# Kernel tuning notes

Measured on AMD Instinct MI355X. Metric: run time of the kernel, lower is better.

The kernel has to match this reference:

```python
import jax, jax.numpy as jnp
import numpy as np

LN_EPS = 1e-5


def setup_inputs() -> dict:
    key = jax.random.key(0)
    ks = jax.random.split(key, 6)
    B, M, N, D = 16, 128, 128, 128
    NM, H = 16, 512
    xav = float(np.sqrt(2.0 / (D + D)))  # xavier_normal over (in_dim, out_dim) fan
    return {
        "x": jax.random.normal(ks[0], (B, M, N, D), jnp.float32),
        "w1": jax.random.normal(ks[1], (D, D, NM, 2), jnp.float32) * xav,
        "w2": jax.random.normal(ks[2], (D, D, NM, 2), jnp.float32) * xav,
        "ff_w0": jax.random.normal(ks[3], (D, H), jnp.float32) * float(1.0 / np.sqrt(D)),
        "ff_b0": jnp.zeros((H,), jnp.float32),
        "ff_w1": jax.random.normal(ks[4], (H, D), jnp.float32) * float(1.0 / np.sqrt(H)),
        "ff_b1": jnp.zeros((D,), jnp.float32),
        "ln_g": jnp.ones((D,), jnp.float32),
        "ln_b": jnp.zeros((D,), jnp.float32),
    }


def _layer_norm(h, g, b):
    mu = jnp.mean(h, axis=-1, keepdims=True)
    var = jnp.mean(jnp.square(h - mu), axis=-1, keepdims=True)
    return (h - mu) * jax.lax.rsqrt(var + LN_EPS) * g + b


def _forward_fourier(x, w1, w2):
    # x: [B, M, N, I] -> [B, I, M, N]
    xt = jnp.transpose(x, (0, 3, 1, 2))
    B, I, M, N = xt.shape
    nm = w1.shape[2]
    cw1 = w1[..., 0] + 1j * w1[..., 1]  # [I, O, nm]
    cw2 = w2[..., 0] + 1j * w2[..., 1]
    O = cw1.shape[1]

    # Fourier along last axis (y)
    fty = jnp.fft.rfft(xt, axis=-1, norm="ortho")                    # [B,I,M,N//2+1]
    f1 = jnp.einsum("bixy,ioy->boxy", fty[..., :nm], cw1)            # [B,O,M,nm]
    pad_y = jnp.zeros((B, O, M, N // 2 + 1 - nm), dtype=f1.dtype)
    xy = jnp.fft.irfft(jnp.concatenate([f1, pad_y], axis=-1), n=N, axis=-1, norm="ortho")

    # Fourier along second-to-last axis (x)
    ftx = jnp.fft.rfft(xt, axis=-2, norm="ortho")                    # [B,I,M//2+1,N]
    f2 = jnp.einsum("bixy,iox->boxy", ftx[:, :, :nm, :], cw2)        # [B,O,nm,N]
    pad_x = jnp.zeros((B, O, M // 2 + 1 - nm, N), dtype=f2.dtype)
    xx = jnp.fft.irfft(jnp.concatenate([f2, pad_x], axis=-2), n=M, axis=-2, norm="ortho")

    return jnp.transpose(xx + xy, (0, 2, 3, 1))  # [B,M,N,O]


def reference(x, w1, w2, ff_w0, ff_b0, ff_w1, ff_b1, ln_g, ln_b):
    h = _forward_fourier(x, w1, w2)
    # backcast FeedForward: Linear -> ReLU -> Linear -> LayerNorm (dropout=0)
    h1 = jax.nn.relu(jnp.einsum("bmni,ih->bmnh", h, ff_w0) + ff_b0)
    h2 = jnp.einsum("bmnh,ho->bmno", h1, ff_w1) + ff_b1
    return _layer_norm(h2, ln_g, ln_b)
```

## Files before the change

kernel.cpp:

```cpp
#include <hip/hip_runtime.h>


#define LN_EPS 1e-5f
#define NMODES 16
#define FROW 4096
#define HROW 16384

typedef __attribute__((ext_vector_type(8))) short short8;
typedef __attribute__((ext_vector_type(8))) ushort ushort8;
typedef __attribute__((ext_vector_type(4))) ushort ushort4v;
typedef __attribute__((ext_vector_type(4))) short short4v;
typedef __attribute__((ext_vector_type(4))) float f32x4;

__device__ __forceinline__ ushort f2bf(float f) {
    unsigned u = __float_as_uint(f);
    unsigned r = (u + 0x7FFFu + ((u >> 16) & 1u)) >> 16;
    return (ushort)r;
}
__device__ __forceinline__ float bf2f(ushort h) {
    return __uint_as_float(((unsigned)h) << 16);
}

__global__ void k_setup(float* __restrict__ Tc, float* __restrict__ Ts,
                        float* __restrict__ IT) {
    const float invs = 0.08838834764831845f;
    for (int idx = threadIdx.x; idx < NMODES * 128; idx += blockDim.x) {
        int k = idx >> 7, n = idx & 127;
        int p = (k * n) & 127;
        float th = (float)p * (6.283185307179586f / 128.0f);
        float c = cosf(th), s = sinf(th);
        Tc[idx] = c * invs;
        Ts[idx] = -s * invs;
        float ck = (k == 0) ? invs : 2.0f * invs;
        IT[n * 32 + 2 * k]     = ck * c;
        IT[n * 32 + 2 * k + 1] = -ck * s;
    }
}

__global__ void k_wpack(const float* __restrict__ w, ushort* __restrict__ Wph,
                        ushort* __restrict__ Wpl) {
    int idx = blockIdx.x * 256 + threadIdx.x;
    int k  = idx >> 16;
    int op = (idx >> 8) & 255;
    int ip = idx & 255;
    int i = ip & 127, o = op & 127;
    const float* base = w + (((i << 7) | o) * NMODES + k) * 2;
    float re = base[0], im = base[1];
    float v = (ip < 128) ? ((op < 128) ? re : im)
                         : ((op < 128) ? -im : re);
    ushort hi = f2bf(v);
    ushort lo = f2bf(v - bf2f(hi));
    Wph[idx] = hi;
    Wpl[idx] = lo;
}

__global__ __launch_bounds__(256) void k_wcvt(const float* __restrict__ w0,
        const float* __restrict__ w1, ushort* __restrict__ w0t,
        ushort* __restrict__ w1t) {
    int idx = blockIdx.x * 256 + threadIdx.x;
    int h = idx >> 7, k = idx & 127;
    w0t[idx] = f2bf(w0[k * 512 + h]);
    int o = idx >> 9, hh = idx & 511;
    w1t[idx] = f2bf(w1[hh * 128 + o]);
}

__global__ __launch_bounds__(128) void k_fft(const float* __restrict__ x,
        const float* __restrict__ Tc, const float* __restrict__ Ts,
        float* __restrict__ F, int mode) {
    __shared__ float Tc_s[NMODES * 128];
    __shared__ float Ts_s[NMODES * 128];
    for (int e = threadIdx.x; e < NMODES * 128; e += 128) {
        Tc_s[e] = Tc[e];
        Ts_s[e] = Ts[e];
    }
    __syncthreads();
    int row = blockIdx.x * 4 + (threadIdx.x >> 5);
    int i0 = (threadIdx.x & 31) * 4;
    size_t base; int ts;
    if (mode == 0) { base = (size_t)row * HROW; ts = 128; }
    else { base = (size_t)(row >> 7) * 2097152 + (size_t)(row & 127) * 128; ts = 16384; }

    f32x4 re[NMODES], im[NMODES];
#pragma unroll
    for (int k = 0; k < NMODES; ++k) {
        re[k] = {0.f, 0.f, 0.f, 0.f};
        im[k] = {0.f, 0.f, 0.f, 0.f};
    }

    f32x4 xv[4];
#pragma unroll
    for (int j = 0; j < 4; ++j)
        xv[j] = *(const f32x4*)(x + base + (size_t)j * ts + i0);

#pragma unroll 1
    for (int tb = 0; tb < 32; ++tb) {
        int t0 = tb * 4;
        f32x4 nx[4];
        if (tb < 31) {
#pragma unroll
            for (int j = 0; j < 4; ++j)
                nx[j] = *(const f32x4*)(x + base + (size_t)(t0 + 4 + j) * ts + i0);
        }
#pragma unroll
        for (int k = 0; k < NMODES; ++k) {
            f32x4 c4 = *(const f32x4*)&Tc_s[k * 128 + t0];
            f32x4 s4 = *(const f32x4*)&Ts_s[k * 128 + t0];
#pragma unroll
            for (int q = 0; q < 4; ++q) {
                re[k][q] += xv[0][q] * c4[0] + xv[1][q] * c4[1]
                          + xv[2][q] * c4[2] + xv[3][q] * c4[3];
                im[k][q] += xv[0][q] * s4[0] + xv[1][q] * s4[1]
                          + xv[2][q] * s4[2] + xv[3][q] * s4[3];
            }
        }
        if (tb < 31) {
#pragma unroll
            for (int j = 0; j < 4; ++j) xv[j] = nx[j];
        }
    }
    float* outp = F + (size_t)row * FROW;
#pragma unroll
    for (int k = 0; k < NMODES; ++k) {
        *(f32x4*)(outp + k * 256 + i0)       = re[k];
        *(f32x4*)(outp + k * 256 + 128 + i0) = im[k];
    }
}

__global__ __launch_bounds__(256) void k_mixm(const float* __restrict__ A,
        const ushort* __restrict__ Wph, const ushort* __restrict__ Wpl,
        float* __restrict__ outF) {
    __shared__ ushort Ah[32 * 264];
    __shared__ ushort Al[32 * 264];
    int tid = threadIdx.x;
    int kt = blockIdx.x & 15;
    int bm0 = (blockIdx.x >> 4) * 32;
    {
        int row = tid >> 3, cg = tid & 7;
        const float* arow = A + (bm0 + row) * FROW + kt * 256 + cg * 32;
        ushort* ah = &Ah[row * 264 + cg * 32];
        ushort* al = &Al[row * 264 + cg * 32];
#pragma unroll
        for (int j = 0; j < 8; ++j) {
            f32x4 v = *(const f32x4*)(arow + j * 4);
            short4v h4, l4;
#pragma unroll
            for (int q = 0; q < 4; ++q) {
                ushort h = f2bf(v[q]);
                h4[q] = (short)h;
                l4[q] = (short)f2bf(v[q] - bf2f(h));
            }
            *(short4v*)(ah + j * 4) = h4;
            *(short4v*)(al + j * 4) = l4;
        }
    }
    __syncthreads();
    int lane = tid & 63, wid = tid >> 6;
    int frow = lane & 15, fk8 = (lane >> 4) * 8, fr4 = (lane >> 4) * 4;
    f32x4 acc[2][4];
#pragma unroll
    for (int a = 0; a < 2; ++a)
#pragma unroll
        for (int c = 0; c < 4; ++c) acc[a][c] = {0.f, 0.f, 0.f, 0.f};
    const ushort* wph = Wph + kt * 65536;
    const ushort* wpl = Wpl + kt * 65536;
#pragma unroll
    for (int kk = 0; kk < 8; ++kk) {
        short8 ah0 = *(const short8*)&Ah[(frow)      * 264 + kk * 32 + fk8];
        short8 ah1 = *(const short8*)&Ah[(16 + frow) * 264 + kk * 32 + fk8];
        short8 al0 = *(const short8*)&Al[(frow)      * 264 + kk * 32 + fk8];
        short8 al1 = *(const short8*)&Al[(16 + frow) * 264 + kk * 32 + fk8];
#pragma unroll
        for (int tc = 0; tc < 4; ++tc) {
            int op = wid * 64 + tc * 16 + frow;
            int base = op * 256 + kk * 32 + fk8;
            short8 wh = *(const short8*)&wph[base];
            short8 wl = *(const short8*)&wpl[base];
            acc[0][tc] = __builtin_amdgcn_mfma_f32_16x16x32_bf16(ah0, wh, acc[0][tc], 0, 0, 0);
            acc[0][tc] = __builtin_amdgcn_mfma_f32_16x16x32_bf16(ah0, wl, acc[0][tc], 0, 0, 0);
            acc[0][tc] = __builtin_amdgcn_mfma_f32_16x16x32_bf16(al0, wh, acc[0][tc], 0, 0, 0);
            acc[1][tc] = __builtin_amdgcn_mfma_f32_16x16x32_bf16(ah1, wh, acc[1][tc], 0, 0, 0);
            acc[1][tc] = __builtin_amdgcn_mfma_f32_16x16x32_bf16(ah1, wl, acc[1][tc], 0, 0, 0);
            acc[1][tc] = __builtin_amdgcn_mfma_f32_16x16x32_bf16(al1, wh, acc[1][tc], 0, 0, 0);
        }
    }
#pragma unroll
    for (int tr = 0; tr < 2; ++tr)
#pragma unroll
        for (int tc = 0; tc < 4; ++tc)
#pragma unroll
            for (int r = 0; r < 4; ++r)
                outF[(bm0 + tr * 16 + fr4 + r) * FROW + kt * 256 + wid * 64 + tc * 16 + frow]
                    = acc[tr][tc][r];
}

__global__ __launch_bounds__(1024) void k_icdft(const float* __restrict__ f,
        const float* __restrict__ IT, ushort* __restrict__ obf,
        float* __restrict__ h32, const ushort* __restrict__ hyin, int mode) {
    __shared__ float IT_s[128 * 32];
    __shared__ float f_s[32 * 128];
    int tid = threadIdx.x;
    int row = blockIdx.x;
    *(f32x4*)&IT_s[tid * 4] = *(const f32x4*)&IT[tid * 4];
    *(f32x4*)&f_s[tid * 4]  = *(const f32x4*)(f + (size_t)row * FROW + tid * 4);
    __syncthreads();
    int og = tid & 31, ng = tid >> 5;
    int o4 = og * 4;

    f32x4 acc[4];
#pragma unroll
    for (int j = 0; j < 4; ++j) acc[j] = {0.f, 0.f, 0.f, 0.f};

#pragma unroll
    for (int kpb = 0; kpb < 8; ++kpb) {
        int kp0 = kpb * 4;
        f32x4 fv0 = *(const f32x4*)&f_s[(kp0 + 0) * 128 + o4];
        f32x4 fv1 = *(const f32x4*)&f_s[(kp0 + 1) * 128 + o4];
        f32x4 fv2 = *(const f32x4*)&f_s[(kp0 + 2) * 128 + o4];
        f32x4 fv3 = *(const f32x4*)&f_s[(kp0 + 3) * 128 + o4];
#pragma unroll
        for (int j = 0; j < 4; ++j) {
            int n = ng * 4 + j;
            f32x4 it = *(const f32x4*)&IT_s[n * 32 + kp0];
#pragma unroll
            for (int q = 0; q < 4; ++q)
                acc[j][q] += fv0[q] * it[0] + fv1[q] * it[1]
                           + fv2[q] * it[2] + fv3[q] * it[3];
        }
    }

    if (mode == 0) {
#pragma unroll
        for (int j = 0; j < 4; ++j) {
            int n = ng * 4 + j;
            ushort4v t;
#pragma unroll
            for (int q = 0; q < 4; ++q) t[q] = f2bf(acc[j][q]);
            *(ushort4v*)&obf[(size_t)row * HROW + n * 128 + o4] = t;
        }
    } else if (mode == 1) {
#pragma unroll
        for (int j = 0; j < 4; ++j) {
            int n = ng * 4 + j;
            *(f32x4*)&h32[(size_t)row * HROW + n * 128 + o4] = acc[j];
        }
    } else if (mode == 2) {
        size_t base = (size_t)(row >> 7) * 2097152 + (size_t)(row & 127) * 128 + o4;
#pragma unroll
        for (int j = 0; j < 4; ++j) {
            int n = ng * 4 + j;
            size_t ix = base + (size_t)n * 16384;
            ushort4v hv = *(const ushort4v*)&hyin[ix];
            ushort4v t;
#pragma unroll
            for (int q = 0; q < 4; ++q) t[q] = f2bf(bf2f(hv[q]) + acc[j][q]);
            *(ushort4v*)&obf[ix] = t;
        }
    } else {
        size_t base = (size_t)(row >> 7) * 2097152 + (size_t)(row & 127) * 128 + o4;
#pragma unroll
        for (int j = 0; j < 4; ++j) {
            int n = ng * 4 + j;
            size_t ix = base + (size_t)n * 16384;
            f32x4 hv = *(const f32x4*)&h32[ix];
            ushort4v t;
#pragma unroll
            for (int q = 0; q < 4; ++q) t[q] = f2bf(hv[q] + acc[j][q]);
            *(ushort4v*)&obf[ix] = t;
        }
    }
}

__global__ __launch_bounds__(256) void k_ffn1(const ushort* __restrict__ hin,
        const ushort* __restrict__ w0t, const float* __restrict__ b0,
        ushort* __restrict__ h1o) {
    __shared__ ushort A_l[128 * 136];
    __shared__ ushort B_l[64 * 136];
    int tid = threadIdx.x;
    int ht = blockIdx.x & 7, rt = blockIdx.x >> 3;
    int R0 = rt * 128, H0 = ht * 64;

#pragma unroll
    for (int i = 0; i < 8; ++i) {
        int e = tid + i * 256;
        int row = e >> 4, c16 = e & 15;
        *(ushort8*)&A_l[row * 136 + c16 * 8] =
            *(const ushort8*)(hin + (size_t)(R0 + row) * 128 + c16 * 8);
    }
#pragma unroll
    for (int i = 0; i < 4; ++i) {
        int e = tid + i * 256;
        int row = e >> 4, c16 = e & 15;
        *(ushort8*)&B_l[row * 136 + c16 * 8] =
            *(const ushort8*)(w0t + (H0 + row) * 128 + c16 * 8);
    }
    __syncthreads();

    int lane = tid & 63, wave = tid >> 6;
    int frow = lane & 15, qg = lane >> 4, fk8 = qg * 8, fr4 = qg * 4;
    int r2 = wave >> 1, c2 = wave & 1;

    f32x4 acc[4][2];
#pragma unroll
    for (int a = 0; a < 4; ++a)
#pragma unroll
        for (int c = 0; c < 2; ++c) acc[a][c] = {0.f, 0.f, 0.f, 0.f};

#pragma unroll
    for (int kk = 0; kk < 4; ++kk) {
        short8 af[4], bf[2];
#pragma unroll
        for (int tr = 0; tr < 4; ++tr)
            af[tr] = *(const short8*)&A_l[(r2 * 64 + tr * 16 + frow) * 136 + kk * 32 + fk8];
#pragma unroll
        for (int tc = 0; tc < 2; ++tc)
            bf[tc] = *(const short8*)&B_l[(c2 * 32 + tc * 16 + frow) * 136 + kk * 32 + fk8];
#pragma unroll
        for (int tr = 0; tr < 4; ++tr)
#pragma unroll
            for (int tc = 0; tc < 2; ++tc)
                acc[tr][tc] = __builtin_amdgcn_mfma_f32_16x16x32_bf16(
                    af[tr], bf[tc], acc[tr][tc], 0, 0, 0);
    }

    float b0v[2];
    b0v[0] = b0[H0 + c2 * 32 + frow];
    b0v[1] = b0[H0 + c2 * 32 + 16 + frow];
#pragma unroll
    for (int tr = 0; tr < 4; ++tr)
#pragma unroll
        for (int tc = 0; tc < 2; ++tc)
#pragma unroll
            for (int r = 0; r < 4; ++r) {
                int row = r2 * 64 + tr * 16 + fr4 + r;
                int col = H0 + c2 * 32 + tc * 16 + frow;
                h1o[(size_t)(R0 + row) * 512 + col] =
                    f2bf(fmaxf(acc[tr][tc][r] + b0v[tc], 0.f));
            }
}

__global__ __launch_bounds__(256) void k_ffn2(const ushort* __restrict__ h1,
        const ushort* __restrict__ w1t, const float* __restrict__ b1,
        const float* __restrict__ g, const float* __restrict__ bb,
        float* __restrict__ out) {
    __shared__ ushort A_l[32 * 72];
    __shared__ ushort B_l[128 * 72];
    __shared__ float ps_s[128];
    __shared__ float pq_s[128];
    int tid = threadIdx.x;
    int R0 = blockIdx.x * 32;
    int lane = tid & 63, wave = tid >> 6;
    int frow = lane & 15, qg = lane >> 4, fk8 = qg * 8, fr4 = qg * 4;
    int sAr = tid >> 3, sc8 = tid & 7;

    *(ushort8*)&A_l[sAr * 72 + sc8 * 8] =
        *(const ushort8*)(h1 + (size_t)(R0 + sAr) * 512 + sc8 * 8);
#pragma unroll
    for (int i = 0; i < 4; ++i) {
        int ro = sAr + i * 32;
        *(ushort8*)&B_l[ro * 72 + sc8 * 8] =
            *(const ushort8*)(w1t + ro * 512 + sc8 * 8);
    }
    __syncthreads();

    f32x4 acc[2][2];
#pragma unroll
    for (int a = 0; a < 2; ++a)
#pragma unroll
        for (int c = 0; c < 2; ++c) acc[a][c] = {0.f, 0.f, 0.f, 0.f};

#pragma unroll 1
    for (int kt = 0; kt < 8; ++kt) {
        ushort8 sa, sb0, sb1, sb2, sb3;
        if (kt < 7) {
            int koff = (kt + 1) * 64 + sc8 * 8;
            sa  = *(const ushort8*)(h1 + (size_t)(R0 + sAr) * 512 + koff);
            sb0 = *(const ushort8*)(w1t + (sAr +  0) * 512 + koff);
            sb1 = *(const ushort8*)(w1t + (sAr + 32) * 512 + koff);
            sb2 = *(const ushort8*)(w1t + (sAr + 64) * 512 + koff);
            sb3 = *(const ushort8*)(w1t + (sAr + 96) * 512 + koff);
        }
#pragma unroll
        for (int kk = 0; kk < 2; ++kk) {
            short8 af[2], bf[2];
#pragma unroll
            for (int tr = 0; tr < 2; ++tr)
                af[tr] = *(const short8*)&A_l[(tr * 16 + frow) * 72 + kk * 32 + fk8];
#pragma unroll
            for (int tc = 0; tc < 2; ++tc)
                bf[tc] = *(const short8*)&B_l[(wave * 32 + tc * 16 + frow) * 72 + kk * 32 + fk8];
#pragma unroll
            for (int tr = 0; tr < 2; ++tr)
#pragma unroll
                for (int tc = 0; tc < 2; ++tc)
                    acc[tr][tc] = __builtin_amdgcn_mfma_f32_16x16x32_bf16(
                        af[tr], bf[tc], acc[tr][tc], 0, 0, 0);
        }
        __syncthreads();
        if (kt < 7) {
            *(ushort8*)&A_l[sAr * 72 + sc8 * 8] = sa;
            *(ushort8*)&B_l[(sAr +  0) * 72 + sc8 * 8] = sb0;
            *(ushort8*)&B_l[(sAr + 32) * 72 + sc8 * 8] = sb1;
            *(ushort8*)&B_l[(sAr + 64) * 72 + sc8 * 8] = sb2;
            *(ushort8*)&B_l[(sAr + 96) * 72 + sc8 * 8] = sb3;
            __syncthreads();
        }
    }

    float b1v[2], gv[2], bv[2];
#pragma unroll
    for (int tc = 0; tc < 2; ++tc) {
        int o = wave * 32 + tc * 16 + frow;
        b1v[tc] = b1[o]; gv[tc] = g[o]; bv[tc] = bb[o];
    }
#pragma unroll
    for (int tr = 0; tr < 2; ++tr)
#pragma unroll
        for (int r = 0; r < 4; ++r) {
            float s = 0.f, qq = 0.f;
#pragma unroll
            for (int tc = 0; tc < 2; ++tc) {
                float v = acc[tr][tc][r] + b1v[tc];
                acc[tr][tc][r] = v;
                s += v; qq += v * v;
            }
            s += __shfl_xor(s, 1); qq += __shfl_xor(qq, 1);
            s += __shfl_xor(s, 2); qq += __shfl_xor(qq, 2);
            s += __shfl_xor(s, 4); qq += __shfl_xor(qq, 4);
            s += __shfl_xor(s, 8); qq += __shfl_xor(qq, 8);
            if (frow == 0) {
                int row = tr * 16 + fr4 + r;
                ps_s[wave * 32 + row] = s;
                pq_s[wave * 32 + row] = qq;
            }
        }
    __syncthreads();
#pragma unroll
    for (int tr = 0; tr < 2; ++tr)
#pragma unroll
        for (int r = 0; r < 4; ++r) {
            int row = tr * 16 + fr4 + r;
            float S = ps_s[row] + ps_s[32 + row] + ps_s[64 + row] + ps_s[96 + row];
            float Q = pq_s[row] + pq_s[32 + row] + pq_s[64 + row] + pq_s[96 + row];
            float mu = S * (1.0f / 128.0f);
            float var = Q * (1.0f / 128.0f) - mu * mu;
            float rs = rsqrtf(fmaxf(var, 0.f) + LN_EPS);
            float* orow = &out[(size_t)(R0 + row) * 128 + wave * 32];
            orow[frow]      = (acc[tr][0][r] - mu) * rs * gv[0] + bv[0];
            orow[16 + frow] = (acc[tr][1][r] - mu) * rs * gv[1] + bv[1];
        }
}

extern "C" void kernel_launch(void* const* d_in, const int* in_sizes, int n_in,
                              void* d_out, int out_size, void* d_ws, size_t ws_size,
                              hipStream_t stream) {
    (void)in_sizes; (void)n_in; (void)out_size;
    const float* x   = (const float*)d_in[0];
    const float* w1  = (const float*)d_in[1];
    const float* w2  = (const float*)d_in[2];
    const float* fw0 = (const float*)d_in[3];
    const float* fb0 = (const float*)d_in[4];
    const float* fw1 = (const float*)d_in[5];
    const float* fb1 = (const float*)d_in[6];
    const float* lng = (const float*)d_in[7];
    const float* lnb = (const float*)d_in[8];
    float* out = (float*)d_out;

    char* ws = (char*)d_ws;
    float*  Tc  = (float*)(ws);
    float*  Ts  = (float*)(ws + 8192);
    float*  IT  = (float*)(ws + 16384);
    ushort* Wph = (ushort*)(ws + 32768);
    ushort* Wpl = (ushort*)(ws + 32768 + 2097152);
    ushort* w0t = (ushort*)(ws + 4227072);
    ushort* w1t = (ushort*)(ws + 4358144);
    float*  buf0 = (float*)(ws + 4489216);
    ushort* hy   = (ushort*)(ws + 38043648);
    ushort* hsum = (ushort*)(ws + 105152512);
    const size_t need_two = 172261376ull;
    int two = (ws_size >= need_two) ? 1 : 0;
    ushort* hbfs = hy;

    k_setup<<<1, 256, 0, stream>>>(Tc, Ts, IT);
    k_wcvt <<<256, 256, 0, stream>>>(fw0, fw1, w0t, w1t);

    k_wpack<<<4096, 256, 0, stream>>>(w1, Wph, Wpl);
    k_fft  <<<512, 128, 0, stream>>>(x, Tc, Ts, buf0, 0);
    k_mixm <<<1024, 256, 0, stream>>>(buf0, Wph, Wpl, buf0);
    if (two) k_icdft<<<2048, 1024, 0, stream>>>(buf0, IT, hy, out, hy, 0);
    else     k_icdft<<<2048, 1024, 0, stream>>>(buf0, IT, hy, out, hy, 1);

    k_wpack<<<4096, 256, 0, stream>>>(w2, Wph, Wpl);
    k_fft  <<<512, 128, 0, stream>>>(x, Tc, Ts, buf0, 1);
    k_mixm <<<1024, 256, 0, stream>>>(buf0, Wph, Wpl, buf0);
    if (two) k_icdft<<<2048, 1024, 0, stream>>>(buf0, IT, hsum, out, hy, 2);
    else     k_icdft<<<2048, 1024, 0, stream>>>(buf0, IT, hbfs, out, hy, 3);

    if (two) {
        for (int c = 0; c < 4; ++c) {
            const size_t off = (size_t)c * 65536 * 128;
            k_ffn1<<<4096, 256, 0, stream>>>(hsum + off, w0t, fb0, hy);
            k_ffn2<<<2048, 256, 0, stream>>>(hy, w1t, fb1, lng, lnb, out + off);
        }
    } else {
        ushort* h1buf = (ushort*)buf0;
        for (int c = 0; c < 8; ++c) {
            const size_t off = (size_t)c * 32768 * 128;
            k_ffn1<<<2048, 256, 0, stream>>>(hbfs + off, w0t, fb0, h1buf);
            k_ffn2<<<1024, 256, 0, stream>>>(h1buf, w1t, fb1, lng, lnb, out + off);
        }
    }
}
```

Before: 540.7 us.

## Compute truncated forward DFT with split-bf16 MFMA instead of scalar FMA

The forward partial DFT (16 modes, cos/sin) becomes a matrix multiply on MFMA 16x16x32 bf16 instructions. The twiddle table is stored as hi/lo bf16 pairs, and each slab of x is split into hi/lo bf16 in LDS, with three MFMAs per tile approximating fp32 accuracy. One block now handles one 128x128 slab instead of four rows per block. This replaces the scalar FMA-bound loop with matrix-core throughput, at the cost of split-precision error, extra LDS traffic and synchronisation.

```diff
diff --git a/kernel.cpp b/kernel.cpp
--- a/kernel.cpp
+++ b/kernel.cpp
@@ -21,19 +21,26 @@
     return __uint_as_float(((unsigned)h) << 16);
 }
 
-__global__ void k_setup(float* __restrict__ Tc, float* __restrict__ Ts,
+__global__ void k_setup(ushort* __restrict__ T2h, ushort* __restrict__ T2l,
                         float* __restrict__ IT) {
     const float invs = 0.08838834764831845f;
+    for (int idx = threadIdx.x; idx < 32 * 128; idx += blockDim.x) {
+        int kp = idx >> 7, n = idx & 127;
+        int k = kp >> 1;
+        int p = (k * n) & 127;
+        float th = (float)p * (6.283185307179586f / 128.0f);
+        float v = (kp & 1) ? (-sinf(th) * invs) : (cosf(th) * invs);
+        ushort hi = f2bf(v);
+        T2h[idx] = hi;
+        T2l[idx] = f2bf(v - bf2f(hi));
+    }
     for (int idx = threadIdx.x; idx < NMODES * 128; idx += blockDim.x) {
         int k = idx >> 7, n = idx & 127;
         int p = (k * n) & 127;
         float th = (float)p * (6.283185307179586f / 128.0f);
-        float c = cosf(th), s = sinf(th);
-        Tc[idx] = c * invs;
-        Ts[idx] = -s * invs;
         float ck = (k == 0) ? invs : 2.0f * invs;
-        IT[n * 32 + 2 * k]     = ck * c;
-        IT[n * 32 + 2 * k + 1] = -ck * s;
+        IT[n * 32 + 2 * k]     = ck * cosf(th);
+        IT[n * 32 + 2 * k + 1] = -ck * sinf(th);
     }
 }
 
@@ -64,66 +71,85 @@
     w1t[idx] = f2bf(w1[hh * 128 + o]);
 }
 
-__global__ __launch_bounds__(128) void k_fft(const float* __restrict__ x,
-        const float* __restrict__ Tc, const float* __restrict__ Ts,
+__global__ __launch_bounds__(256) void k_fft(const float* __restrict__ x,
+        const ushort* __restrict__ T2h, const ushort* __restrict__ T2l,
         float* __restrict__ F, int mode) {
-    __shared__ float Tc_s[NMODES * 128];
-    __shared__ float Ts_s[NMODES * 128];
-    for (int e = threadIdx.x; e < NMODES * 128; e += 128) {
-        Tc_s[e] = Tc[e];
-        Ts_s[e] = Ts[e];
-    }
-    __syncthreads();
-    int row = blockIdx.x * 4 + (threadIdx.x >> 5);
-    int i0 = (threadIdx.x & 31) * 4;
+    __shared__ ushort Xh[128 * 38];
+    __shared__ ushort Xl[128 * 38];
+    int tid = threadIdx.x;
+    int slab = blockIdx.x;
     size_t base; int ts;
-    if (mode == 0) { base = (size_t)row * HROW; ts = 128; }
-    else { base = (size_t)(row >> 7) * 2097152 + (size_t)(row & 127) * 128; ts = 16384; }
-
-    f32x4 re[NMODES], im[NMODES];
-#pragma unroll
-    for (int k = 0; k < NMODES; ++k) {
-        re[k] = {0.f, 0.f, 0.f, 0.f};
-        im[k] = {0.f, 0.f, 0.f, 0.f};
-    }
-
-    f32x4 xv[4];
-#pragma unroll
-    for (int j = 0; j < 4; ++j)
-        xv[j] = *(const f32x4*)(x + base + (size_t)j * ts + i0);
+    if (mode == 0) { base = (size_t)slab * HROW; ts = 128; }
+    else { base = (size_t)(slab >> 7) * 2097152 + (size_t)(slab & 127) * 128; ts = 16384; }
+
+    int sr2 = tid >> 4, sc = tid & 15;
+    int lane = tid & 63, w = tid >> 6;
+    int frow = lane & 15, fk8 = (lane >> 4) * 8, fr4 = (lane >> 4) * 4;
+
+    f32x4 acc[2][2];
+#pragma unroll
+    for (int a = 0; a < 2; ++a)
+#pragma unroll
+        for (int c = 0; c < 2; ++c) acc[a][c] = {0.f, 0.f, 0.f, 0.f};
 
 #pragma unroll 1
-    for (int tb = 0; tb < 32; ++tb) {
-        int t0 = tb * 4;
-        f32x4 nx[4];
-        if (tb < 31) {
-#pragma unroll
-            for (int j = 0; j < 4; ++j)
-                nx[j] = *(const f32x4*)(x + base + (size_t)(t0 + 4 + j) * ts + i0);
-        }
-#pragma unroll
-        for (int k = 0; k < NMODES; ++k) {
-            f32x4 c4 = *(const f32x4*)&Tc_s[k * 128 + t0];
-            f32x4 s4 = *(const f32x4*)&Ts_s[k * 128 + t0];
-#pragma unroll
-            for (int q = 0; q < 4; ++q) {
-                re[k][q] += xv[0][q] * c4[0] + xv[1][q] * c4[1]
-                          + xv[2][q] * c4[2] + xv[3][q] * c4[3];
-                im[k][q] += xv[0][q] * s4[0] + xv[1][q] * s4[1]
-                          + xv[2][q] * s4[2] + xv[3][q] * s4[3];
+    for (int nc = 0; nc < 4; ++nc) {
+        if (nc) __syncthreads();
+        {
+            const float* pa = x + base + (size_t)(nc * 32 + 2 * sr2) * ts + sc * 8;
+            const float* pb = pa + ts;
+            f32x4 a0 = *(const f32x4*)pa;
+            f32x4 a1 = *(const f32x4*)(pa + 4);
+            f32x4 b0 = *(const f32x4*)pb;
+            f32x4 b1 = *(const f32x4*)(pb + 4);
+            uint* xh32 = (uint*)Xh;
+            uint* xl32 = (uint*)Xl;
+#pragma unroll
+            for (int q = 0; q < 8; ++q) {
+                float av = (q < 4) ? a0[q] : a1[q - 4];
+                float bv = (q < 4) ? b0[q] : b1[q - 4];
+                ushort ah = f2bf(av), bh = f2bf(bv);
+                ushort al = f2bf(av - bf2f(ah)), bl = f2bf(bv - bf2f(bh));
+                int i = sc * 8 + q;
+                xh32[i * 19 + sr2] = (uint)ah | ((uint)bh << 16);
+                xl32[i * 19 + sr2] = (uint)al | ((uint)bl << 16);
             }
         }
-        if (tb < 31) {
-#pragma unroll
-            for (int j = 0; j < 4; ++j) xv[j] = nx[j];
-        }
-    }
-    float* outp = F + (size_t)row * FROW;
-#pragma unroll
-    for (int k = 0; k < NMODES; ++k) {
-        *(f32x4*)(outp + k * 256 + i0)       = re[k];
-        *(f32x4*)(outp + k * 256 + 128 + i0) = im[k];
-    }
+        __syncthreads();
+        short8 ah_[2], al_[2], bh_[2], bl_[2];
+#pragma unroll
+        for (int kt = 0; kt < 2; ++kt) {
+            int ro = (kt * 16 + frow) * 128 + nc * 32 + fk8;
+            ah_[kt] = *(const short8*)&T2h[ro];
+            al_[kt] = *(const short8*)&T2l[ro];
+        }
+#pragma unroll
+        for (int it = 0; it < 2; ++it) {
+            int i = w * 32 + it * 16 + frow;
+            bh_[it] = *(const short8*)&Xh[i * 38 + fk8];
+            bl_[it] = *(const short8*)&Xl[i * 38 + fk8];
+        }
+#pragma unroll
+        for (int kt = 0; kt < 2; ++kt)
+#pragma unroll
+            for (int it = 0; it < 2; ++it) {
+                acc[kt][it] = __builtin_amdgcn_mfma_f32_16x16x32_bf16(
+                    ah_[kt], bh_[it], acc[kt][it], 0, 0, 0);
+                acc[kt][it] = __builtin_amdgcn_mfma_f32_16x16x32_bf16(
+                    ah_[kt], bl_[it], acc[kt][it], 0, 0, 0);
+                acc[kt][it] = __builtin_amdgcn_mfma_f32_16x16x32_bf16(
+                    al_[kt], bh_[it], acc[kt][it], 0, 0, 0);
+            }
+    }
+
+    float* outp = F + (size_t)slab * FROW;
+#pragma unroll
+    for (int kt = 0; kt < 2; ++kt)
+#pragma unroll
+        for (int it = 0; it < 2; ++it)
+#pragma unroll
+            for (int r = 0; r < 4; ++r)
+                outp[(kt * 16 + fr4 + r) * 128 + w * 32 + it * 16 + frow] = acc[kt][it][r];
 }
 
 __global__ __launch_bounds__(256) void k_mixm(const float* __restrict__ A,
@@ -466,8 +492,8 @@
     float* out = (float*)d_out;
 
     char* ws = (char*)d_ws;
-    float*  Tc  = (float*)(ws);
-    float*  Ts  = (float*)(ws + 8192);
+    ushort* T2h = (ushort*)(ws);
+    ushort* T2l = (ushort*)(ws + 8192);
     float*  IT  = (float*)(ws + 16384);
     ushort* Wph = (ushort*)(ws + 32768);
     ushort* Wpl = (ushort*)(ws + 32768 + 2097152);
@@ -480,17 +506,17 @@
     int two = (ws_size >= need_two) ? 1 : 0;
     ushort* hbfs = hy;
 
-    k_setup<<<1, 256, 0, stream>>>(Tc, Ts, IT);
+    k_setup<<<1, 256, 0, stream>>>(T2h, T2l, IT);
     k_wcvt <<<256, 256, 0, stream>>>(fw0, fw1, w0t, w1t);
 
     k_wpack<<<4096, 256, 0, stream>>>(w1, Wph, Wpl);
-    k_fft  <<<512, 128, 0, stream>>>(x, Tc, Ts, buf0, 0);
+    k_fft  <<<2048, 256, 0, stream>>>(x, T2h, T2l, buf0, 0);
     k_mixm <<<1024, 256, 0, stream>>>(buf0, Wph, Wpl, buf0);
     if (two) k_icdft<<<2048, 1024, 0, stream>>>(buf0, IT, hy, out, hy, 0);
     else     k_icdft<<<2048, 1024, 0, stream>>>(buf0, IT, hy, out, hy, 1);
 
     k_wpack<<<4096, 256, 0, stream>>>(w2, Wph, Wpl);
-    k_fft  <<<512, 128, 0, stream>>>(x, Tc, Ts, buf0, 1);
+    k_fft  <<<2048, 256, 0, stream>>>(x, T2h, T2l, buf0, 1);
     k_mixm <<<1024, 256, 0, stream>>>(buf0, Wph, Wpl, buf0);
     if (two) k_icdft<<<2048, 1024, 0, stream>>>(buf0, IT, hsum, out, hy, 2);
     else     k_icdft<<<2048, 1024, 0, stream>>>(buf0, IT, hbfs, out, hy, 3);
```

Result: faster. 502.0 us (-7.1%).
